# Kernel tuning notes

Measured on AMD Instinct MI355X. Metric: run time of the kernel, lower is better.

The kernel has to match this reference:

```python
import jax, jax.numpy as jnp
import numpy as np

B, T, C, H = 2, 2048, 1024, 16
D = C // H  # head dim = 64
EPS = 1e-5


def layernorm(x, g, b):
    mu = jnp.mean(x, axis=-1, keepdims=True)
    var = jnp.var(x, axis=-1, keepdims=True)
    return (x - mu) * jax.lax.rsqrt(var + EPS) * g + b


def setup_inputs() -> dict:
    key = jax.random.key(0)
    ks = jax.random.split(key, 8)
    init_scale = 0.25
    return {
        "x": jax.random.normal(ks[0], (B, T, C), dtype=jnp.float32),
        # weights stored [in, out] (transpose of torch Linear)
        "w_qkv": jax.random.normal(ks[1], (C, 3 * C), dtype=jnp.float32) * init_scale,
        "b_qkv": jnp.zeros((3 * C,), dtype=jnp.float32),
        "w_proj": jax.random.normal(ks[2], (C, C), dtype=jnp.float32) * init_scale,
        "b_proj": jnp.zeros((C,), dtype=jnp.float32),
        "ln1_g": jnp.ones((C,), dtype=jnp.float32),
        "ln1_b": jnp.zeros((C,), dtype=jnp.float32),
        "w_fc": jax.random.normal(ks[3], (C, 4 * C), dtype=jnp.float32) * init_scale,
        "b_fc": jnp.zeros((4 * C,), dtype=jnp.float32),
        "w_out": jax.random.normal(ks[4], (4 * C, C), dtype=jnp.float32) * init_scale,
        "b_out": jnp.zeros((C,), dtype=jnp.float32),
        "ln2_g": jnp.ones((C,), dtype=jnp.float32),
        "ln2_b": jnp.zeros((C,), dtype=jnp.float32),
    }


def reference(x, w_qkv, b_qkv, w_proj, b_proj, ln1_g, ln1_b,
              w_fc, b_fc, w_out, b_out, ln2_g, ln2_b):
    # ---- attention sub-block (pre-LN) ----
    h = layernorm(x, ln1_g, ln1_b)
    qkv = h @ w_qkv + b_qkv                      # [B,T,3C]
    q, k, v = jnp.split(qkv, 3, axis=-1)
    q = q.reshape(B, T, H, D)
    k = k.reshape(B, T, H, D)
    v = v.reshape(B, T, H, D)
    scores = jnp.einsum('bthd,bshd->bhts', q, k) * (1.0 / np.sqrt(D))
    attn = jax.nn.softmax(scores, axis=-1)       # full [B,H,T,T] as in source
    out = jnp.einsum('bhts,bshd->bthd', attn, v).reshape(B, T, C)
    x = x + out @ w_proj + b_proj
    # ---- MLP sub-block (pre-LN) ----
    h = layernorm(x, ln2_g, ln2_b)
    h = jax.nn.gelu(h @ w_fc + b_fc, approximate=False)  # torch nn.GELU default = exact
    x = x + h @ w_out + b_out
    return x
```

## Files before the change

### kernel.cpp

```cpp
#include <hip/hip_runtime.h>
#include <hip/hip_bf16.h>
#include <math.h>

#define DEVINL static __device__ __forceinline__

typedef _Float16 f16x8 __attribute__((ext_vector_type(8)));
typedef _Float16 f16x4 __attribute__((ext_vector_type(4)));
typedef float f32x4 __attribute__((ext_vector_type(4)));

constexpr int TT = 2048, CC = 1024, HH = 16, DD = 64;

DEVINL void gload_lds16(const void* g, void* s) {
  __builtin_amdgcn_global_load_lds(
      (const __attribute__((address_space(1))) void*)g,
      (__attribute__((address_space(3))) void*)s, 16, 0, 0);
}

__global__ __launch_bounds__(256) void transpose_cast(
    const float* __restrict__ in, _Float16* __restrict__ out, int K, int N) {
  __shared__ float tile[32][33];
  int n0 = blockIdx.x * 32, k0 = blockIdx.y * 32;
  int tx = threadIdx.x & 31, ty = threadIdx.x >> 5;
  #pragma unroll
  for (int i = 0; i < 32; i += 8)
    tile[ty + i][tx] = in[(size_t)(k0 + ty + i) * N + n0 + tx];
  __syncthreads();
  #pragma unroll
  for (int i = 0; i < 32; i += 8)
    out[(size_t)(n0 + ty + i) * K + k0 + tx] = (_Float16)tile[tx][ty + i];
}

__global__ __launch_bounds__(256) void ln_cast(
    const float* __restrict__ x, const float* __restrict__ g,
    const float* __restrict__ bta, _Float16* __restrict__ out) {
  int row = blockIdx.x, t = threadIdx.x;
  float4 v = ((const float4*)(x + (size_t)row * CC))[t];
  float s = v.x + v.y + v.z + v.w;
  float s2 = v.x * v.x + v.y * v.y + v.z * v.z + v.w * v.w;
  #pragma unroll
  for (int o = 32; o >= 1; o >>= 1) { s += __shfl_xor(s, o); s2 += __shfl_xor(s2, o); }
  __shared__ float ss[4], ssq[4];
  int w = t >> 6;
  if ((t & 63) == 0) { ss[w] = s; ssq[w] = s2; }
  __syncthreads();
  s = ss[0] + ss[1] + ss[2] + ss[3];
  s2 = ssq[0] + ssq[1] + ssq[2] + ssq[3];
  float mu = s * (1.0f / CC);
  float rs = rsqrtf(s2 * (1.0f / CC) - mu * mu + 1e-5f);
  float4 gv = ((const float4*)g)[t];
  float4 bv = ((const float4*)bta)[t];
  f16x4 o4;
  o4[0] = (_Float16)((v.x - mu) * rs * gv.x + bv.x);
  o4[1] = (_Float16)((v.y - mu) * rs * gv.y + bv.y);
  o4[2] = (_Float16)((v.z - mu) * rs * gv.z + bv.z);
  o4[3] = (_Float16)((v.w - mu) * rs * gv.w + bv.w);
  ((f16x4*)(out + (size_t)row * CC))[t] = o4;
}

template <int EPI, int N, int K, int BN>
__global__ __launch_bounds__(256) void gemm_bt(
    const _Float16* __restrict__ A, const _Float16* __restrict__ Bt,
    const float* __restrict__ bias, const float* __restrict__ res,
    void* __restrict__ outp) {
  constexpr int NWN = BN / 64;
  constexpr int MI = 2 * NWN;
  __shared__ __align__(16) _Float16 As[128 * 64];
  __shared__ __align__(16) _Float16 Bs[BN * 64];
  const int bm0 = blockIdx.y * 128, bn0 = blockIdx.x * BN;
  const int t = threadIdx.x, w = t >> 6, l = t & 63, lg = l >> 4, lr = l & 15;
  const int wr = w / NWN, wc = w % NWN;
  const int srow = t >> 3, sc = t & 7;
  f32x4 acc[MI][4] = {};
  for (int k0 = 0; k0 < K; k0 += 64) {
    #pragma unroll
    for (int q = 0; q < 4; ++q) {
      int row = q * 32 + srow;
      int gc = sc ^ (row & 7);
      gload_lds16(A + (size_t)(bm0 + row) * K + k0 + gc * 8, As + row * 64 + sc * 8);
    }
    #pragma unroll
    for (int q = 0; q < BN / 32; ++q) {
      int row = q * 32 + srow;
      int gc = sc ^ (row & 7);
      gload_lds16(Bt + (size_t)(bn0 + row) * K + k0 + gc * 8, Bs + row * 64 + sc * 8);
    }
    __syncthreads();
    #pragma unroll
    for (int ks = 0; ks < 2; ++ks) {
      f16x8 af[MI], bfr[4];
      #pragma unroll
      for (int mi = 0; mi < MI; ++mi) {
        int row = wr * (16 * MI) + mi * 16 + lr;
        af[mi] = *(const f16x8*)(As + row * 64 + (((ks * 4 + lg) ^ (row & 7)) << 3));
      }
      #pragma unroll
      for (int ni = 0; ni < 4; ++ni) {
        int row = wc * 64 + ni * 16 + lr;
        bfr[ni] = *(const f16x8*)(Bs + row * 64 + (((ks * 4 + lg) ^ (row & 7)) << 3));
      }
      #pragma unroll
      for (int mi = 0; mi < MI; ++mi)
        #pragma unroll
        for (int ni = 0; ni < 4; ++ni)
          acc[mi][ni] = __builtin_amdgcn_mfma_f32_16x16x32_f16(af[mi], bfr[ni], acc[mi][ni], 0, 0, 0);
    }
    __syncthreads();
  }
  #pragma unroll
  for (int mi = 0; mi < MI; ++mi) {
    #pragma unroll
    for (int ni = 0; ni < 4; ++ni) {
      int gc = bn0 + wc * 64 + ni * 16 + lr;
      float bv = bias[gc];
      #pragma unroll
      for (int r = 0; r < 4; ++r) {
        int gr = bm0 + wr * (16 * MI) + mi * 16 + lg * 4 + r;
        float v = acc[mi][ni][r] + bv;
        if constexpr (EPI == 1) {
          float gl = 0.5f * v * (1.0f + erff(v * 0.70710678118654752f));
          ((_Float16*)outp)[(size_t)gr * N + gc] = (_Float16)gl;
        } else {
          ((float*)outp)[(size_t)gr * N + gc] = res[(size_t)gr * N + gc] + v;
        }
      }
    }
  }
}

__global__ __launch_bounds__(256) void gemm_qkv(
    const _Float16* __restrict__ A, const _Float16* __restrict__ Bt,
    const float* __restrict__ bias,
    _Float16* __restrict__ qo, _Float16* __restrict__ ko,
    _Float16* __restrict__ vt) {
  __shared__ __align__(16) _Float16 As[128 * 64];
  __shared__ __align__(16) _Float16 Bs[128 * 64];
  const int bm0 = blockIdx.y * 128, bn0 = blockIdx.x * 128;
  const int t = threadIdx.x, w = t >> 6, l = t & 63, lg = l >> 4, lr = l & 15;
  const int wr = w >> 1, wc = w & 1;
  const int srow = t >> 3, sc = t & 7;
  f32x4 acc[4][4] = {};
  for (int k0 = 0; k0 < 1024; k0 += 64) {
    #pragma unroll
    for (int q = 0; q < 4; ++q) {
      int row = q * 32 + srow;
      int gc = sc ^ (row & 7);
      gload_lds16(A + (size_t)(bm0 + row) * 1024 + k0 + gc * 8, As + row * 64 + sc * 8);
      gload_lds16(Bt + (size_t)(bn0 + row) * 1024 + k0 + gc * 8, Bs + row * 64 + sc * 8);
    }
    __syncthreads();
    #pragma unroll
    for (int ks = 0; ks < 2; ++ks) {
      f16x8 af[4], bfr[4];
      #pragma unroll
      for (int mi = 0; mi < 4; ++mi) {
        int row = wr * 64 + mi * 16 + lr;
        af[mi] = *(const f16x8*)(As + row * 64 + (((ks * 4 + lg) ^ (row & 7)) << 3));
      }
      #pragma unroll
      for (int ni = 0; ni < 4; ++ni) {
        int row = wc * 64 + ni * 16 + lr;
        bfr[ni] = *(const f16x8*)(Bs + row * 64 + (((ks * 4 + lg) ^ (row & 7)) << 3));
      }
      #pragma unroll
      for (int mi = 0; mi < 4; ++mi)
        #pragma unroll
        for (int ni = 0; ni < 4; ++ni)
          acc[mi][ni] = __builtin_amdgcn_mfma_f32_16x16x32_f16(af[mi], bfr[ni], acc[mi][ni], 0, 0, 0);
    }
    __syncthreads();
  }
  const float QSCL = 0.125f * 1.44269504f;
  #pragma unroll
  for (int mi = 0; mi < 4; ++mi) {
    #pragma unroll
    for (int ni = 0; ni < 4; ++ni) {
      int gc = bn0 + wc * 64 + ni * 16 + lr;
      float bv = bias[gc];
      int sec = gc >> 10, cc = gc & 1023;
      #pragma unroll
      for (int r = 0; r < 4; ++r) {
        int gr = bm0 + wr * 64 + mi * 16 + lg * 4 + r;
        float v = acc[mi][ni][r] + bv;
        if (sec == 0) {
          qo[(size_t)gr * 1024 + cc] = (_Float16)(v * QSCL);
        } else if (sec == 1) {
          ko[(size_t)gr * 1024 + cc] = (_Float16)v;
        } else {
          int hh = cc >> 6, dd = cc & 63;
          int bb = gr >> 11, tk = gr & (TT - 1);
          vt[(((size_t)bb * HH + hh) * DD + dd) * TT + tk] = (_Float16)v;
        }
      }
    }
  }
}

__global__ __launch_bounds__(256, 4) void flash_attn(
    const _Float16* __restrict__ qg, const _Float16* __restrict__ kg,
    const _Float16* __restrict__ vt, _Float16* __restrict__ att) {
  const int qt0 = blockIdx.x * 64, h = blockIdx.y, b = blockIdx.z;
  const int t = threadIdx.x, w = t >> 6, l = t & 63, lg = l >> 4, lr = l & 15;
  __shared__ __align__(16) _Float16 Ks[2][64 * 64];
  __shared__ __align__(16) _Float16 VTs[2][64 * 64];
  __shared__ __align__(16) _Float16 Ps[4][16 * 64];
  const int srow = t >> 3, sc = t & 7;
  const int gcs = sc ^ (srow & 7);
  const int dk0 = srow * 64 + sc * 8;
  const _Float16* kg_b = kg + ((size_t)b * TT + srow) * CC + h * DD + gcs * 8;
  const _Float16* vt_b = vt + (((size_t)b * HH + h) * DD + srow) * TT + gcs * 8;
  int fro[2][4], pfo[2], pwo[4][4];
  #pragma unroll
  for (int ks = 0; ks < 2; ++ks) {
    #pragma unroll
    for (int ni = 0; ni < 4; ++ni) {
      int row = ni * 16 + lr;
      fro[ks][ni] = row * 64 + (((ks * 4 + lg) ^ (row & 7)) << 3);
    }
    pfo[ks] = lr * 64 + (((ks * 4 + lg) ^ (lr & 7)) << 3);
  }
  #pragma unroll
  for (int r = 0; r < 4; ++r) {
    int prow = lg * 4 + r, rx = prow & 7;
    #pragma unroll
    for (int ni = 0; ni < 4; ++ni)
      pwo[r][ni] = prow * 64 + (((2 * ni + (lr >> 3)) ^ rx) << 3) + (lr & 7);
  }
  f16x8 qf[2];
  #pragma unroll
  for (int ks = 0; ks < 2; ++ks)
    qf[ks] = *(const f16x8*)(qg + ((size_t)(b * TT + qt0 + w * 16 + lr)) * CC +
                             h * DD + ks * 32 + lg * 8);
  f32x4 o[4] = {};
  f32x4 osum = {};
  float mrow[4];
  #pragma unroll
  for (int r = 0; r < 4; ++r) mrow[r] = -3.0e38f;
  const f16x8 ones = {(_Float16)1, (_Float16)1, (_Float16)1, (_Float16)1,
                      (_Float16)1, (_Float16)1, (_Float16)1, (_Float16)1};

  auto STAGE = [&](int bufi, int kv0) {
    #pragma unroll
    for (int q = 0; q < 2; ++q) {
      gload_lds16(kg_b + (size_t)(kv0 + q * 32) * CC, Ks[bufi] + q * 2048 + dk0);
      gload_lds16(vt_b + q * 32 * TT + kv0, VTs[bufi] + q * 2048 + dk0);
    }
  };
  STAGE(0, 0);
  __syncthreads();
  int cur = 0;
  for (int kv0 = 0; kv0 < TT; kv0 += 64) {
    if (kv0 + 64 < TT) STAGE(cur ^ 1, kv0 + 64);
    const _Float16* Kc = Ks[cur];
    const _Float16* Vc = VTs[cur];
    f32x4 s[4] = {};
    __builtin_amdgcn_s_setprio(1);
    #pragma unroll
    for (int ks = 0; ks < 2; ++ks)
      #pragma unroll
      for (int ni = 0; ni < 4; ++ni) {
        f16x8 kf = *(const f16x8*)(Kc + fro[ks][ni]);
        s[ni] = __builtin_amdgcn_mfma_f32_16x16x32_f16(qf[ks], kf, s[ni], 0, 0, 0);
      }
    __builtin_amdgcn_s_setprio(0);
    float m4[4];
    int ok = 1;
    #pragma unroll
    for (int r = 0; r < 4; ++r) {
      m4[r] = fmaxf(fmaxf(s[0][r], s[1][r]), fmaxf(s[2][r], s[3][r]));
      ok &= (m4[r] <= mrow[r] + 8.0f) ? 1 : 0;
    }
    if (!__all(ok)) {
      #pragma unroll
      for (int r = 0; r < 4; ++r) {
        float rm = m4[r];
        #pragma unroll
        for (int msk = 1; msk <= 8; msk <<= 1) rm = fmaxf(rm, __shfl_xor(rm, msk));
        float mn = fmaxf(mrow[r], rm);
        float corr = exp2f(mrow[r] - mn);
        mrow[r] = mn;
        #pragma unroll
        for (int di = 0; di < 4; ++di) o[di][r] *= corr;
        osum[r] *= corr;
      }
    }
    _Float16* Pw = Ps[w];
    #pragma unroll
    for (int r = 0; r < 4; ++r) {
      Pw[pwo[r][0]] = (_Float16)exp2f(s[0][r] - mrow[r]);
      Pw[pwo[r][1]] = (_Float16)exp2f(s[1][r] - mrow[r]);
      Pw[pwo[r][2]] = (_Float16)exp2f(s[2][r] - mrow[r]);
      Pw[pwo[r][3]] = (_Float16)exp2f(s[3][r] - mrow[r]);
    }
    __builtin_amdgcn_s_setprio(1);
    #pragma unroll
    for (int ks = 0; ks < 2; ++ks) {
      f16x8 pf = *(const f16x8*)(Pw + pfo[ks]);
      #pragma unroll
      for (int di = 0; di < 4; ++di) {
        f16x8 vf = *(const f16x8*)(Vc + fro[ks][di]);
        o[di] = __builtin_amdgcn_mfma_f32_16x16x32_f16(pf, vf, o[di], 0, 0, 0);
      }
      osum = __builtin_amdgcn_mfma_f32_16x16x32_f16(pf, ones, osum, 0, 0, 0);
    }
    __builtin_amdgcn_s_setprio(0);
    __syncthreads();
    cur ^= 1;
  }
  #pragma unroll
  for (int r = 0; r < 4; ++r) {
    float rinv = 1.0f / osum[r];
    int row_g = qt0 + w * 16 + lg * 4 + r;
    #pragma unroll
    for (int di = 0; di < 4; ++di)
      att[((size_t)(b * TT + row_g)) * CC + h * DD + di * 16 + lr] =
          (_Float16)(o[di][r] * rinv);
  }
}

extern "C" void kernel_launch(void* const* d_in, const int* in_sizes, int n_in,
                              void* d_out, int out_size, void* d_ws, size_t ws_size,
                              hipStream_t stream) {
  const float* x      = (const float*)d_in[0];
  const float* w_qkv  = (const float*)d_in[1];
  const float* b_qkv  = (const float*)d_in[2];
  const float* w_proj = (const float*)d_in[3];
  const float* b_proj = (const float*)d_in[4];
  const float* ln1_g  = (const float*)d_in[5];
  const float* ln1_b  = (const float*)d_in[6];
  const float* w_fc   = (const float*)d_in[7];
  const float* b_fc   = (const float*)d_in[8];
  const float* w_out  = (const float*)d_in[9];
  const float* b_out  = (const float*)d_in[10];
  const float* ln2_g  = (const float*)d_in[11];
  const float* ln2_b  = (const float*)d_in[12];

  char* ws = (char*)d_ws;
  _Float16* wqkv_t = (_Float16*)(ws);
  _Float16* wproj_t= (_Float16*)(ws + 6291456);
  _Float16* wfc_t  = (_Float16*)(ws + 8388608);
  _Float16* wout_t = (_Float16*)(ws + 16777216);
  _Float16* hslot  = (_Float16*)(ws + 25165824);
  _Float16* qbuf   = (_Float16*)(ws + 33554432);
  _Float16* kbuf   = (_Float16*)(ws + 41943040);
  _Float16* vtbuf  = (_Float16*)(ws + 50331648);
  _Float16* tbuf   = (_Float16*)(ws + 33554432);
  float*    x1     = (float*)(ws + 67108864);

  transpose_cast<<<dim3(96, 32), 256, 0, stream>>>(w_qkv, wqkv_t, 1024, 3072);
  transpose_cast<<<dim3(32, 32), 256, 0, stream>>>(w_proj, wproj_t, 1024, 1024);
  transpose_cast<<<dim3(128, 32), 256, 0, stream>>>(w_fc, wfc_t, 1024, 4096);
  transpose_cast<<<dim3(32, 128), 256, 0, stream>>>(w_out, wout_t, 4096, 1024);

  ln_cast<<<4096, 256, 0, stream>>>(x, ln1_g, ln1_b, hslot);
  gemm_qkv<<<dim3(24, 32), 256, 0, stream>>>(hslot, wqkv_t, b_qkv, qbuf, kbuf, vtbuf);
  flash_attn<<<dim3(32, 16, 2), 256, 0, stream>>>(qbuf, kbuf, vtbuf, hslot);
  gemm_bt<2, 1024, 1024, 64><<<dim3(16, 32), 256, 0, stream>>>(hslot, wproj_t, b_proj, x, x1);
  ln_cast<<<4096, 256, 0, stream>>>(x1, ln2_g, ln2_b, hslot);
  gemm_bt<1, 4096, 1024, 128><<<dim3(32, 32), 256, 0, stream>>>(hslot, wfc_t, b_fc, nullptr, tbuf);
  gemm_bt<2, 1024, 4096, 64><<<dim3(16, 32), 256, 0, stream>>>(tbuf, wout_t, b_out, x1, (float*)d_out);
}
```

Baseline: 313.2 us.

## Load K and V fragments directly from global memory in flash attention

Removes the double-buffered LDS staging of K and V tiles and the per-iteration block barrier. Each wave now reads its K and V^T MFMA fragments straight from global memory, 32 keys per iteration, and keeps only a small per-wave LDS buffer for P. This cuts LDS traffic and synchronisation, but the four waves of a block no longer share K/V loads, so global/L2 traffic rises. Global load latency is also exposed with no software prefetch.

After: 448.7 us. 1.43x slower.

```diff
diff --git a/kernel.cpp b/kernel.cpp
--- a/kernel.cpp
+++ b/kernel.cpp
@@ -195,36 +195,24 @@
   }
 }
 
-__global__ __launch_bounds__(256, 4) void flash_attn(
+__global__ __launch_bounds__(256) void flash_attn(
     const _Float16* __restrict__ qg, const _Float16* __restrict__ kg,
     const _Float16* __restrict__ vt, _Float16* __restrict__ att) {
   const int qt0 = blockIdx.x * 64, h = blockIdx.y, b = blockIdx.z;
   const int t = threadIdx.x, w = t >> 6, l = t & 63, lg = l >> 4, lr = l & 15;
-  __shared__ __align__(16) _Float16 Ks[2][64 * 64];
-  __shared__ __align__(16) _Float16 VTs[2][64 * 64];
-  __shared__ __align__(16) _Float16 Ps[4][16 * 64];
-  const int srow = t >> 3, sc = t & 7;
-  const int gcs = sc ^ (srow & 7);
-  const int dk0 = srow * 64 + sc * 8;
-  const _Float16* kg_b = kg + ((size_t)b * TT + srow) * CC + h * DD + gcs * 8;
-  const _Float16* vt_b = vt + (((size_t)b * HH + h) * DD + srow) * TT + gcs * 8;
-  int fro[2][4], pfo[2], pwo[4][4];
-  #pragma unroll
-  for (int ks = 0; ks < 2; ++ks) {
-    #pragma unroll
-    for (int ni = 0; ni < 4; ++ni) {
-      int row = ni * 16 + lr;
-      fro[ks][ni] = row * 64 + (((ks * 4 + lg) ^ (row & 7)) << 3);
-    }
-    pfo[ks] = lr * 64 + (((ks * 4 + lg) ^ (lr & 7)) << 3);
-  }
+  __shared__ __align__(16) _Float16 Ps[4][16 * 32];
+  _Float16* Pw = Ps[w];
+  const _Float16* kg_b = kg + ((size_t)b * TT + lr) * CC + h * DD + lg * 8;
+  const _Float16* vt_b = vt + (((size_t)b * HH + h) * DD + lr) * TT + lg * 8;
+  int pwo[4][2];
   #pragma unroll
   for (int r = 0; r < 4; ++r) {
-    int prow = lg * 4 + r, rx = prow & 7;
-    #pragma unroll
-    for (int ni = 0; ni < 4; ++ni)
-      pwo[r][ni] = prow * 64 + (((2 * ni + (lr >> 3)) ^ rx) << 3) + (lr & 7);
-  }
+    int prow = lg * 4 + r, rx = prow & 3;
+    #pragma unroll
+    for (int ni = 0; ni < 2; ++ni)
+      pwo[r][ni] = prow * 32 + (((ni * 2 + (lr >> 3)) ^ rx) << 3) + (lr & 7);
+  }
+  const int pro = lr * 32 + ((lg ^ (lr & 3)) << 3);
   f16x8 qf[2];
   #pragma unroll
   for (int ks = 0; ks < 2; ++ks)
@@ -238,35 +226,26 @@
   const f16x8 ones = {(_Float16)1, (_Float16)1, (_Float16)1, (_Float16)1,
                       (_Float16)1, (_Float16)1, (_Float16)1, (_Float16)1};
 
-  auto STAGE = [&](int bufi, int kv0) {
-    #pragma unroll
-    for (int q = 0; q < 2; ++q) {
-      gload_lds16(kg_b + (size_t)(kv0 + q * 32) * CC, Ks[bufi] + q * 2048 + dk0);
-      gload_lds16(vt_b + q * 32 * TT + kv0, VTs[bufi] + q * 2048 + dk0);
-    }
-  };
-  STAGE(0, 0);
-  __syncthreads();
-  int cur = 0;
-  for (int kv0 = 0; kv0 < TT; kv0 += 64) {
-    if (kv0 + 64 < TT) STAGE(cur ^ 1, kv0 + 64);
-    const _Float16* Kc = Ks[cur];
-    const _Float16* Vc = VTs[cur];
-    f32x4 s[4] = {};
-    __builtin_amdgcn_s_setprio(1);
-    #pragma unroll
-    for (int ks = 0; ks < 2; ++ks)
-      #pragma unroll
-      for (int ni = 0; ni < 4; ++ni) {
-        f16x8 kf = *(const f16x8*)(Kc + fro[ks][ni]);
-        s[ni] = __builtin_amdgcn_mfma_f32_16x16x32_f16(qf[ks], kf, s[ni], 0, 0, 0);
-      }
-    __builtin_amdgcn_s_setprio(0);
+  for (int kv0 = 0; kv0 < TT; kv0 += 32) {
+    const _Float16* kp = kg_b + (size_t)kv0 * CC;
+    f16x8 kf00 = *(const f16x8*)(kp);
+    f16x8 kf01 = *(const f16x8*)(kp + 16 * CC);
+    f16x8 kf10 = *(const f16x8*)(kp + 32);
+    f16x8 kf11 = *(const f16x8*)(kp + 16 * CC + 32);
+    f16x8 vf[4];
+    #pragma unroll
+    for (int di = 0; di < 4; ++di)
+      vf[di] = *(const f16x8*)(vt_b + (size_t)(di * 16) * TT + kv0);
+    f32x4 s0 = {}, s1 = {};
+    s0 = __builtin_amdgcn_mfma_f32_16x16x32_f16(qf[0], kf00, s0, 0, 0, 0);
+    s1 = __builtin_amdgcn_mfma_f32_16x16x32_f16(qf[0], kf01, s1, 0, 0, 0);
+    s0 = __builtin_amdgcn_mfma_f32_16x16x32_f16(qf[1], kf10, s0, 0, 0, 0);
+    s1 = __builtin_amdgcn_mfma_f32_16x16x32_f16(qf[1], kf11, s1, 0, 0, 0);
     float m4[4];
     int ok = 1;
     #pragma unroll
     for (int r = 0; r < 4; ++r) {
-      m4[r] = fmaxf(fmaxf(s[0][r], s[1][r]), fmaxf(s[2][r], s[3][r]));
+      m4[r] = fmaxf(s0[r], s1[r]);
       ok &= (m4[r] <= mrow[r] + 8.0f) ? 1 : 0;
     }
     if (!__all(ok)) {
@@ -283,28 +262,16 @@
         osum[r] *= corr;
       }
     }
-    _Float16* Pw = Ps[w];
     #pragma unroll
     for (int r = 0; r < 4; ++r) {
-      Pw[pwo[r][0]] = (_Float16)exp2f(s[0][r] - mrow[r]);
-      Pw[pwo[r][1]] = (_Float16)exp2f(s[1][r] - mrow[r]);
-      Pw[pwo[r][2]] = (_Float16)exp2f(s[2][r] - mrow[r]);
-      Pw[pwo[r][3]] = (_Float16)exp2f(s[3][r] - mrow[r]);
-    }
-    __builtin_amdgcn_s_setprio(1);
-    #pragma unroll
-    for (int ks = 0; ks < 2; ++ks) {
-      f16x8 pf = *(const f16x8*)(Pw + pfo[ks]);
-      #pragma unroll
-      for (int di = 0; di < 4; ++di) {
-        f16x8 vf = *(const f16x8*)(Vc + fro[ks][di]);
-        o[di] = __builtin_amdgcn_mfma_f32_16x16x32_f16(pf, vf, o[di], 0, 0, 0);
-      }
-      osum = __builtin_amdgcn_mfma_f32_16x16x32_f16(pf, ones, osum, 0, 0, 0);
-    }
-    __builtin_amdgcn_s_setprio(0);
-    __syncthreads();
-    cur ^= 1;
+      Pw[pwo[r][0]] = (_Float16)exp2f(s0[r] - mrow[r]);
+      Pw[pwo[r][1]] = (_Float16)exp2f(s1[r] - mrow[r]);
+    }
+    f16x8 pf = *(const f16x8*)(Pw + pro);
+    #pragma unroll
+    for (int di = 0; di < 4; ++di)
+      o[di] = __builtin_amdgcn_mfma_f32_16x16x32_f16(pf, vf[di], o[di], 0, 0, 0);
+    osum = __builtin_amdgcn_mfma_f32_16x16x32_f16(pf, ones, osum, 0, 0, 0);
   }
   #pragma unroll
   for (int r = 0; r < 4; ++r) {
```

## Rewrite flash attention with 32x32 MFMA and register-resident P

Applied to the files above, without the earlier changes.

The attention kernel moves from 16x16x32 to 32x32x16 MFMA tiles, computing S transposed so each lane holds a full query column. Softmax probabilities are packed into fp16 in registers and exchanged across half-waves with shuffles, which removes the LDS round-trip for P and the extra MFMA for row sums. Each block now covers 128 query rows instead of 64, halving the grid and doubling K/V reuse per LDS load, and launch bounds drop occupancy to 2. It risks higher register pressure and fewer waves to hide latency.

Result: faster. 300.8 us (-4.0%).

```diff
diff --git a/kernel.cpp b/kernel.cpp
--- a/kernel.cpp
+++ b/kernel.cpp
@@ -7,6 +7,7 @@
 typedef _Float16 f16x8 __attribute__((ext_vector_type(8)));
 typedef _Float16 f16x4 __attribute__((ext_vector_type(4)));
 typedef float f32x4 __attribute__((ext_vector_type(4)));
+typedef float f32x16 __attribute__((ext_vector_type(16)));
 
 constexpr int TT = 2048, CC = 1024, HH = 16, DD = 64;
 
@@ -14,6 +15,13 @@
   __builtin_amdgcn_global_load_lds(
       (const __attribute__((address_space(1))) void*)g,
       (__attribute__((address_space(3))) void*)s, 16, 0, 0);
+}
+
+DEVINL unsigned pkrtz(float a, float b) {
+  typedef __fp16 hf2 __attribute__((ext_vector_type(2)));
+  union { hf2 h; unsigned u; } c;
+  c.h = __builtin_amdgcn_cvt_pkrtz(a, b);
+  return c.u;
 }
 
 __global__ __launch_bounds__(256) void transpose_cast(
@@ -195,54 +203,36 @@
   }
 }
 
-__global__ __launch_bounds__(256, 4) void flash_attn(
+__global__ __launch_bounds__(256, 2) void flash_attn(
     const _Float16* __restrict__ qg, const _Float16* __restrict__ kg,
     const _Float16* __restrict__ vt, _Float16* __restrict__ att) {
-  const int qt0 = blockIdx.x * 64, h = blockIdx.y, b = blockIdx.z;
-  const int t = threadIdx.x, w = t >> 6, l = t & 63, lg = l >> 4, lr = l & 15;
+  const int qt0 = blockIdx.x * 128, h = blockIdx.y, b = blockIdx.z;
+  const int t = threadIdx.x, w = t >> 6, l = t & 63;
+  const int l31 = l & 31, hi = l >> 5;
   __shared__ __align__(16) _Float16 Ks[2][64 * 64];
   __shared__ __align__(16) _Float16 VTs[2][64 * 64];
-  __shared__ __align__(16) _Float16 Ps[4][16 * 64];
   const int srow = t >> 3, sc = t & 7;
   const int gcs = sc ^ (srow & 7);
-  const int dk0 = srow * 64 + sc * 8;
   const _Float16* kg_b = kg + ((size_t)b * TT + srow) * CC + h * DD + gcs * 8;
   const _Float16* vt_b = vt + (((size_t)b * HH + h) * DD + srow) * TT + gcs * 8;
-  int fro[2][4], pfo[2], pwo[4][4];
-  #pragma unroll
-  for (int ks = 0; ks < 2; ++ks) {
-    #pragma unroll
-    for (int ni = 0; ni < 4; ++ni) {
-      int row = ni * 16 + lr;
-      fro[ks][ni] = row * 64 + (((ks * 4 + lg) ^ (row & 7)) << 3);
-    }
-    pfo[ks] = lr * 64 + (((ks * 4 + lg) ^ (lr & 7)) << 3);
-  }
-  #pragma unroll
-  for (int r = 0; r < 4; ++r) {
-    int prow = lg * 4 + r, rx = prow & 7;
-    #pragma unroll
-    for (int ni = 0; ni < 4; ++ni)
-      pwo[r][ni] = prow * 64 + (((2 * ni + (lr >> 3)) ^ rx) << 3) + (lr & 7);
-  }
-  f16x8 qf[2];
-  #pragma unroll
-  for (int ks = 0; ks < 2; ++ks)
-    qf[ks] = *(const f16x8*)(qg + ((size_t)(b * TT + qt0 + w * 16 + lr)) * CC +
-                             h * DD + ks * 32 + lg * 8);
-  f32x4 o[4] = {};
-  f32x4 osum = {};
-  float mrow[4];
-  #pragma unroll
-  for (int r = 0; r < 4; ++r) mrow[r] = -3.0e38f;
-  const f16x8 ones = {(_Float16)1, (_Float16)1, (_Float16)1, (_Float16)1,
-                      (_Float16)1, (_Float16)1, (_Float16)1, (_Float16)1};
+  const int dst0 = srow * 64 + sc * 8;
+
+  f16x8 qf[4];
+  {
+    const _Float16* qp = qg + ((size_t)(b * TT + qt0 + w * 32 + l31)) * CC + h * DD + hi * 8;
+    #pragma unroll
+    for (int ks = 0; ks < 4; ++ks) qf[ks] = *(const f16x8*)(qp + ks * 16);
+  }
+  const int rx = l31 & 7;
+
+  f32x16 o0 = {}, o1 = {};
+  float osum = 0.0f, mrow = -3.0e38f;
 
   auto STAGE = [&](int bufi, int kv0) {
     #pragma unroll
-    for (int q = 0; q < 2; ++q) {
-      gload_lds16(kg_b + (size_t)(kv0 + q * 32) * CC, Ks[bufi] + q * 2048 + dk0);
-      gload_lds16(vt_b + q * 32 * TT + kv0, VTs[bufi] + q * 2048 + dk0);
+    for (int qq = 0; qq < 2; ++qq) {
+      gload_lds16(kg_b + (size_t)(kv0 + qq * 32) * CC, Ks[bufi] + qq * 2048 + dst0);
+      gload_lds16(vt_b + qq * 32 * TT + kv0, VTs[bufi] + qq * 2048 + dst0);
     }
   };
   STAGE(0, 0);
@@ -252,68 +242,82 @@
     if (kv0 + 64 < TT) STAGE(cur ^ 1, kv0 + 64);
     const _Float16* Kc = Ks[cur];
     const _Float16* Vc = VTs[cur];
-    f32x4 s[4] = {};
-    __builtin_amdgcn_s_setprio(1);
-    #pragma unroll
-    for (int ks = 0; ks < 2; ++ks)
-      #pragma unroll
-      for (int ni = 0; ni < 4; ++ni) {
-        f16x8 kf = *(const f16x8*)(Kc + fro[ks][ni]);
-        s[ni] = __builtin_amdgcn_mfma_f32_16x16x32_f16(qf[ks], kf, s[ni], 0, 0, 0);
-      }
-    __builtin_amdgcn_s_setprio(0);
-    float m4[4];
-    int ok = 1;
-    #pragma unroll
-    for (int r = 0; r < 4; ++r) {
-      m4[r] = fmaxf(fmaxf(s[0][r], s[1][r]), fmaxf(s[2][r], s[3][r]));
-      ok &= (m4[r] <= mrow[r] + 8.0f) ? 1 : 0;
-    }
-    if (!__all(ok)) {
-      #pragma unroll
-      for (int r = 0; r < 4; ++r) {
-        float rm = m4[r];
+    #pragma unroll
+    for (int sub = 0; sub < 2; ++sub) {
+      f32x16 s = {};
+      __builtin_amdgcn_s_setprio(1);
+      #pragma unroll
+      for (int ks = 0; ks < 4; ++ks) {
+        int row = sub * 32 + l31;
+        f16x8 kf = *(const f16x8*)(Kc + row * 64 + (((ks * 2 + hi) ^ rx) << 3));
+        s = __builtin_amdgcn_mfma_f32_32x32x16_f16(kf, qf[ks], s, 0, 0, 0);
+      }
+      __builtin_amdgcn_s_setprio(0);
+      float m16 = s[0];
+      #pragma unroll
+      for (int r = 1; r < 16; ++r) m16 = fmaxf(m16, s[r]);
+      int ok = (m16 <= mrow + 8.0f) ? 1 : 0;
+      if (!__all(ok)) {
+        float mo = fmaxf(m16, __shfl_xor(m16, 32));
+        float mn = fmaxf(mrow, mo);
+        float corr = exp2f(mrow - mn);
+        mrow = mn;
         #pragma unroll
-        for (int msk = 1; msk <= 8; msk <<= 1) rm = fmaxf(rm, __shfl_xor(rm, msk));
-        float mn = fmaxf(mrow[r], rm);
-        float corr = exp2f(mrow[r] - mn);
-        mrow[r] = mn;
-        #pragma unroll
-        for (int di = 0; di < 4; ++di) o[di][r] *= corr;
-        osum[r] *= corr;
-      }
-    }
-    _Float16* Pw = Ps[w];
-    #pragma unroll
-    for (int r = 0; r < 4; ++r) {
-      Pw[pwo[r][0]] = (_Float16)exp2f(s[0][r] - mrow[r]);
-      Pw[pwo[r][1]] = (_Float16)exp2f(s[1][r] - mrow[r]);
-      Pw[pwo[r][2]] = (_Float16)exp2f(s[2][r] - mrow[r]);
-      Pw[pwo[r][3]] = (_Float16)exp2f(s[3][r] - mrow[r]);
-    }
-    __builtin_amdgcn_s_setprio(1);
-    #pragma unroll
-    for (int ks = 0; ks < 2; ++ks) {
-      f16x8 pf = *(const f16x8*)(Pw + pfo[ks]);
-      #pragma unroll
-      for (int di = 0; di < 4; ++di) {
-        f16x8 vf = *(const f16x8*)(Vc + fro[ks][di]);
-        o[di] = __builtin_amdgcn_mfma_f32_16x16x32_f16(pf, vf, o[di], 0, 0, 0);
-      }
-      osum = __builtin_amdgcn_mfma_f32_16x16x32_f16(pf, ones, osum, 0, 0, 0);
-    }
-    __builtin_amdgcn_s_setprio(0);
+        for (int r = 0; r < 16; ++r) { o0[r] *= corr; o1[r] *= corr; }
+        osum *= corr;
+      }
+      float p[16];
+      float psum = 0.0f;
+      #pragma unroll
+      for (int r = 0; r < 16; ++r) { p[r] = exp2f(s[r] - mrow); psum += p[r]; }
+      osum += psum;
+      unsigned W[8], X[8];
+      #pragma unroll
+      for (int i = 0; i < 8; ++i) {
+        W[i] = pkrtz(p[2 * i], p[2 * i + 1]);
+        X[i] = __shfl_xor(W[i], 32);
+      }
+      union { unsigned u[4]; f16x8 v; } bp[2];
+      #pragma unroll
+      for (int s2 = 0; s2 < 2; ++s2) {
+        bp[s2].u[0] = hi ? X[4 * s2 + 2] : W[4 * s2 + 0];
+        bp[s2].u[1] = hi ? X[4 * s2 + 3] : W[4 * s2 + 1];
+        bp[s2].u[2] = hi ? W[4 * s2 + 2] : X[4 * s2 + 0];
+        bp[s2].u[3] = hi ? W[4 * s2 + 3] : X[4 * s2 + 1];
+      }
+      __builtin_amdgcn_s_setprio(1);
+      #pragma unroll
+      for (int s2 = 0; s2 < 2; ++s2) {
+        int c = sub * 4 + s2 * 2 + hi;
+        {
+          int row = l31;
+          f16x8 vf = *(const f16x8*)(Vc + row * 64 + ((c ^ rx) << 3));
+          o0 = __builtin_amdgcn_mfma_f32_32x32x16_f16(vf, bp[s2].v, o0, 0, 0, 0);
+        }
+        {
+          int row = 32 + l31;
+          f16x8 vf = *(const f16x8*)(Vc + row * 64 + ((c ^ rx) << 3));
+          o1 = __builtin_amdgcn_mfma_f32_32x32x16_f16(vf, bp[s2].v, o1, 0, 0, 0);
+        }
+      }
+      __builtin_amdgcn_s_setprio(0);
+    }
     __syncthreads();
     cur ^= 1;
   }
-  #pragma unroll
-  for (int r = 0; r < 4; ++r) {
-    float rinv = 1.0f / osum[r];
-    int row_g = qt0 + w * 16 + lg * 4 + r;
-    #pragma unroll
-    for (int di = 0; di < 4; ++di)
-      att[((size_t)(b * TT + row_g)) * CC + h * DD + di * 16 + lr] =
-          (_Float16)(o[di][r] * rinv);
+  osum += __shfl_xor(osum, 32);
+  float rinv = 1.0f / osum;
+  _Float16* ob = att + ((size_t)(b * TT + qt0 + w * 32 + l31)) * CC + h * DD;
+  #pragma unroll
+  for (int i = 0; i < 4; ++i) {
+    int col0 = 8 * i + 4 * hi;
+    uint2 v0, v1;
+    v0.x = pkrtz(o0[4 * i + 0] * rinv, o0[4 * i + 1] * rinv);
+    v0.y = pkrtz(o0[4 * i + 2] * rinv, o0[4 * i + 3] * rinv);
+    v1.x = pkrtz(o1[4 * i + 0] * rinv, o1[4 * i + 1] * rinv);
+    v1.y = pkrtz(o1[4 * i + 2] * rinv, o1[4 * i + 3] * rinv);
+    *(uint2*)(ob + col0) = v0;
+    *(uint2*)(ob + 32 + col0) = v1;
   }
 }
 
@@ -353,7 +357,7 @@
 
   ln_cast<<<4096, 256, 0, stream>>>(x, ln1_g, ln1_b, hslot);
   gemm_qkv<<<dim3(24, 32), 256, 0, stream>>>(hslot, wqkv_t, b_qkv, qbuf, kbuf, vtbuf);
-  flash_attn<<<dim3(32, 16, 2), 256, 0, stream>>>(qbuf, kbuf, vtbuf, hslot);
+  flash_attn<<<dim3(16, 16, 2), 256, 0, stream>>>(qbuf, kbuf, vtbuf, hslot);
   gemm_bt<2, 1024, 1024, 64><<<dim3(16, 32), 256, 0, stream>>>(hslot, wproj_t, b_proj, x, x1);
   ln_cast<<<4096, 256, 0, stream>>>(x1, ln2_g, ln2_b, hslot);
   gemm_bt<1, 4096, 1024, 128><<<dim3(32, 32), 256, 0, stream>>>(hslot, wfc_t, b_fc, nullptr, tbuf);
```
